# Optimization experiments

Measured on AMD Instinct MI355X. Metric: run time of the kernel, lower is better.

Reference implementation:

```python
import jax, jax.numpy as jnp
import numpy as np

N = 100000      # num_nodes
E = 600000      # edges per relation
R = 3           # num_relations
F_IN = 128
F_OUT = 64


def setup_inputs() -> dict:
    key = jax.random.key(0)
    k0, k1, k2, k3 = jax.random.split(key, 4)
    x = jax.random.normal(k0, (N, F_IN), dtype=jnp.float32)
    edge_indices = jax.random.randint(k1, (R, 2, E), 0, N, dtype=jnp.int32)
    # torch.randperm per relation -> fixed permutations as int inputs
    perms = jnp.stack([jax.random.permutation(jax.random.fold_in(k2, r), N).astype(jnp.int32)
                       for r in range(R)])
    # GCNConv glorot weight + zero bias, one per relation
    Ws = jax.random.normal(k3, (R, F_IN, F_OUT), dtype=jnp.float32) * (1.0 / np.sqrt(F_IN))
    bs = jnp.zeros((R, F_OUT), dtype=jnp.float32)
    return {"x": x, "edge_indices": edge_indices, "perms": perms, "Ws": Ws, "bs": bs}


def gcn_conv(h, src, dst, W, b, n):
    """PyG GCNConv: add self-loops, sym-normalize, linear, scatter-sum, bias."""
    loops = jnp.arange(n, dtype=src.dtype)
    s = jnp.concatenate([src, loops])
    d = jnp.concatenate([dst, loops])
    deg = jax.ops.segment_sum(jnp.ones_like(s, dtype=h.dtype), d, num_segments=n)
    dinv = jnp.where(deg > 0, jax.lax.rsqrt(deg), 0.0)
    norm = dinv[s] * dinv[d]                      # [E+n]
    hw = h @ W                                    # [n, F_OUT]
    out = jax.ops.segment_sum(hw[s] * norm[:, None], d, num_segments=n)
    return out + b


def reference(x, edge_indices, perms, Ws, bs):
    # Eval mode: F.dropout(p=0.5, training=False) is identity.
    n = x.shape[0]
    pos_hs, neg_hs, summaries = [], [], []
    for r in range(R):
        src, dst = edge_indices[r, 0], edge_indices[r, 1]
        pos_h = jax.nn.relu(gcn_conv(x, src, dst, Ws[r], bs[r], n))
        neg_h = jax.nn.relu(gcn_conv(x[perms[r]], src, dst, Ws[r], bs[r], n))
        pos_hs.append(pos_h)
        neg_hs.append(neg_h)
        summaries.append(pos_h.mean(axis=0, keepdims=True))
    return (jnp.stack(pos_hs), jnp.stack(neg_hs), jnp.stack(summaries))
```

## Files before the change

### kernel.cpp

```cpp
#include <hip/hip_runtime.h>

#define F_IN 128
#define F_OUT 64
#define NCHUNK 256

typedef float f32x2 __attribute__((ext_vector_type(2)));
typedef float f32x4 __attribute__((ext_vector_type(4)));
typedef short bf16x8 __attribute__((ext_vector_type(8)));

__device__ __forceinline__ unsigned short f2bf(float f) {
    unsigned int u = __float_as_uint(f);
    u += 0x7fff + ((u >> 16) & 1);
    return (unsigned short)(u >> 16);
}
__device__ __forceinline__ float bf2f(unsigned short s) {
    return __uint_as_float((unsigned int)s << 16);
}

__global__ __launch_bounds__(256) void prep_kernel(const int* __restrict__ ei,
                                                   const int* __restrict__ perm,
                                                   const float* __restrict__ W,
                                                   int* __restrict__ deg,
                                                   int* __restrict__ ip,
                                                   unsigned short* __restrict__ wt_hi,
                                                   unsigned short* __restrict__ wt_lo,
                                                   int N, int E, int R,
                                                   int degB, int invB) {
    int b = blockIdx.x;
    if (b < degB) {
        int idx = b * 256 + threadIdx.x;
        if (idx < R * E) {
            int r = idx / E, e = idx - r * E;
            int d = ei[(size_t)r * 2 * E + E + e];
            atomicAdd(&deg[(size_t)r * N + d], 1);
        }
    } else if (b < degB + invB) {
        int idx = (b - degB) * 256 + threadIdx.x;
        if (idx < R * N) {
            int r = idx / N, i = idx - r * N;
            ip[(size_t)r * N + perm[idx]] = i;
        }
    } else {
        int idx = (b - degB - invB) * 256 + threadIdx.x;
        if (idx < R * 64 * 128) {
            int k = idx & 127, c = (idx >> 7) & 63, r = idx >> 13;
            float v = W[((size_t)r * F_IN + k) * F_OUT + c];
            unsigned short h = f2bf(v);
            wt_hi[idx] = h;
            wt_lo[idx] = f2bf(v - bf2f(h));
        }
    }
}

__global__ __launch_bounds__(256) void scan_partial(const int* __restrict__ deg,
                                                    int* __restrict__ psum,
                                                    int N, int chunk) {
    int b = blockIdx.x;
    int r = b >> 8, c = b & 255;
    int start = c * chunk, end = min(start + chunk, N);
    int s = 0;
    for (int i = start + threadIdx.x; i < end; i += 256)
        s += deg[(size_t)r * N + i];
    __shared__ int ls[256];
    ls[threadIdx.x] = s;
    __syncthreads();
    for (int off = 128; off > 0; off >>= 1) {
        if (threadIdx.x < off) ls[threadIdx.x] += ls[threadIdx.x + off];
        __syncthreads();
    }
    if (threadIdx.x == 0) psum[b] = ls[0];
}

__global__ __launch_bounds__(256) void scan_apply2(int* __restrict__ deg,
                                                   const int* __restrict__ psum,
                                                   int* __restrict__ rowstart,
                                                   float* __restrict__ dinv,
                                                   int N, int chunk) {
    int b = blockIdx.x;
    int r = b >> 8, c = b & 255;
    int tid = threadIdx.x, lane = tid & 63, wv = tid >> 6;
    __shared__ int incl[256];
    __shared__ int wsum[4];

    int pv = psum[(r << 8) + tid];
    int sc = pv;
    #pragma unroll
    for (int off = 1; off < 64; off <<= 1) {
        int t = __shfl_up(sc, off, 64);
        if (lane >= off) sc += t;
    }
    if (lane == 63) wsum[wv] = sc;
    __syncthreads();
    int woff = 0;
    for (int w = 0; w < wv; ++w) woff += wsum[w];
    incl[tid] = woff + sc;
    __syncthreads();
    int base = (c == 0) ? 0 : incl[c - 1];
    if (c == 0 && tid == 0)
        rowstart[(size_t)r * (N + 1) + N] = incl[255];

    int start = c * chunk, end = min(start + chunk, N);
    int* dg = deg + (size_t)r * N;
    int* rs = rowstart + (size_t)r * (N + 1);
    float* dv = dinv + (size_t)r * N;
    int v[4]; int tsum = 0;
    #pragma unroll
    for (int j = 0; j < 4; ++j) {
        int idx = start + tid * 4 + j;
        v[j] = (idx < end) ? dg[idx] : 0;
        tsum += v[j];
    }
    int sc2 = tsum;
    #pragma unroll
    for (int off = 1; off < 64; off <<= 1) {
        int t = __shfl_up(sc2, off, 64);
        if (lane >= off) sc2 += t;
    }
    if (lane == 63) wsum[wv] = sc2;
    __syncthreads();
    int woff2 = 0;
    for (int w = 0; w < wv; ++w) woff2 += wsum[w];
    int excl = base + woff2 + sc2 - tsum;
    #pragma unroll
    for (int j = 0; j < 4; ++j) {
        int idx = start + tid * 4 + j;
        if (idx < end) {
            rs[idx] = excl;
            dg[idx] = excl;
            dv[idx] = rsqrtf((float)(v[j] + 1));
        }
        excl += v[j];
    }
}

__global__ __launch_bounds__(256) void fill_gemm(const int* __restrict__ ei,
                                                 const float* __restrict__ dinv,
                                                 int* __restrict__ cursor,
                                                 int2* __restrict__ csr,
                                                 const float* __restrict__ x,
                                                 const unsigned short* __restrict__ wt_hi,
                                                 const unsigned short* __restrict__ wt_lo,
                                                 const int* __restrict__ ip,
                                                 unsigned short* __restrict__ combined,
                                                 int N, int E, int R, int gemmB) {
    constexpr int KP = 136;
    __shared__ __align__(16) unsigned short xs_hi[64 * KP];
    __shared__ __align__(16) unsigned short xs_lo[64 * KP];
    int b = blockIdx.x;

    if (b >= gemmB) {
        int idx = (b - gemmB) * 256 + threadIdx.x;
        if (idx >= R * E) return;
        int r = idx / E, e = idx - r * E;
        const int* base = ei + (size_t)r * 2 * E;
        int s = base[e], d = base[E + e];
        const float* dv = dinv + (size_t)r * N;
        float nrm = dv[s] * dv[d];
        int pos = atomicAdd(&cursor[(size_t)r * N + d], 1);
        int2 sp; sp.x = s; sp.y = __float_as_int(nrm);
        csr[(size_t)r * E + pos] = sp;
        return;
    }

    int row0 = b * 64;
    int tid = threadIdx.x;
    {
        int rr = tid >> 2, q = tid & 3;
        int grow = row0 + rr; if (grow >= N) grow = N - 1;
        const float* xr = x + (size_t)grow * F_IN + q * 32;
        unsigned short* dh = &xs_hi[rr * KP + q * 32];
        unsigned short* dl = &xs_lo[rr * KP + q * 32];
        #pragma unroll
        for (int c = 0; c < 32; c += 4) {
            float4 v = *(const float4*)(xr + c);
            unsigned short h0 = f2bf(v.x), h1 = f2bf(v.y),
                           h2 = f2bf(v.z), h3 = f2bf(v.w);
            ushort4 hv; hv.x = h0; hv.y = h1; hv.z = h2; hv.w = h3;
            *(ushort4*)(dh + c) = hv;
            ushort4 lv;
            lv.x = f2bf(v.x - bf2f(h0)); lv.y = f2bf(v.y - bf2f(h1));
            lv.z = f2bf(v.z - bf2f(h2)); lv.w = f2bf(v.w - bf2f(h3));
            *(ushort4*)(dl + c) = lv;
        }
    }
    __syncthreads();

    int wv = tid >> 6, lane = tid & 63;
    int l15 = lane & 15, lhi = lane >> 4;
    int nbase = wv * 16;
    for (int r = 0; r < R; ++r) {
        f32x4 acc[4];
        #pragma unroll
        for (int ct = 0; ct < 4; ++ct) acc[ct] = (f32x4){0.f, 0.f, 0.f, 0.f};
        const unsigned short* wh = wt_hi + (size_t)r * 64 * 128;
        const unsigned short* wl = wt_lo + (size_t)r * 64 * 128;
        #pragma unroll
        for (int kc = 0; kc < 4; ++kc) {
            int kb = kc * 32 + lhi * 8;
            int ro = (nbase + l15) * KP + kb;
            bf16x8 bh = *(const bf16x8*)&xs_hi[ro];
            bf16x8 bl = *(const bf16x8*)&xs_lo[ro];
            bf16x8 ah[4], al[4];
            #pragma unroll
            for (int ct = 0; ct < 4; ++ct) {
                int wo = (ct * 16 + l15) * 128 + kb;
                ah[ct] = *(const bf16x8*)(wh + wo);
                al[ct] = *(const bf16x8*)(wl + wo);
            }
            #pragma unroll
            for (int ct = 0; ct < 4; ++ct) {
                acc[ct] = __builtin_amdgcn_mfma_f32_16x16x32_bf16(ah[ct], bh, acc[ct], 0, 0, 0);
                acc[ct] = __builtin_amdgcn_mfma_f32_16x16x32_bf16(ah[ct], bl, acc[ct], 0, 0, 0);
                acc[ct] = __builtin_amdgcn_mfma_f32_16x16x32_bf16(al[ct], bh, acc[ct], 0, 0, 0);
            }
        }
        const int* ipr = ip + (size_t)r * N;
        size_t rb = (size_t)r * N;
        int xrow = row0 + nbase + l15;
        if (xrow < N) {
            int nrow = ipr[xrow];
            #pragma unroll
            for (int ct = 0; ct < 4; ++ct) {
                f32x4 a = acc[ct];
                ushort4 v;
                v.x = f2bf(a.x); v.y = f2bf(a.y);
                v.z = f2bf(a.z); v.w = f2bf(a.w);
                int cb = ct * 16 + lhi * 4;
                *(ushort4*)(combined + (rb + xrow) * 128 + cb) = v;
                *(ushort4*)(combined + (rb + nrow) * 128 + 64 + cb) = v;
            }
        }
    }
}

__global__ __launch_bounds__(256) void gather_kernel(const int2* __restrict__ csr,
                                                     const int* __restrict__ rowstart,
                                                     const float* __restrict__ dinv,
                                                     const unsigned short* __restrict__ combined,
                                                     const float* __restrict__ bs,
                                                     float* __restrict__ out_pos,
                                                     float* __restrict__ out_neg,
                                                     float* __restrict__ partial,
                                                     int N, int E) {
    int r = blockIdx.y;
    int lane = threadIdx.x & 63, wv = threadIdx.x >> 6;
    int i = blockIdx.x * 4 + wv;
    i = __builtin_amdgcn_readfirstlane(i);
    int c0 = (lane & 31) * 2;
    __shared__ float ls[4][64];
    float p0 = 0.f, p1 = 0.f;
    if (i < N) {
        const unsigned short* cw = combined + (size_t)r * N * 128;
        const int* rs = rowstart + (size_t)r * (N + 1);
        int j0 = rs[i], j1 = rs[i + 1];
        j0 = __builtin_amdgcn_readfirstlane(j0);
        j1 = __builtin_amdgcn_readfirstlane(j1);
        float di = dinv[(size_t)r * N + i];
        float w = di * di;
        unsigned int sv = *(const unsigned int*)(cw + (size_t)i * 128 + 2 * lane);
        float acc0 = bf2f((unsigned short)sv) * w;
        float acc1 = bf2f((unsigned short)(sv >> 16)) * w;
        const int2* cs = csr + (size_t)r * E;
        int last = j1 - 1;
        for (int j = j0; j < j1; j += 8) {
            int2 e[8];
            float nm[8];
            #pragma unroll
            for (int k = 0; k < 8; ++k) {
                int idx = j + k;
                int ic = idx < last ? idx : last;
                e[k] = cs[ic];
                nm[k] = (idx < j1) ? __int_as_float(e[k].y) : 0.f;
            }
            #pragma unroll
            for (int k = 0; k < 8; ++k) {
                unsigned int v = *(const unsigned int*)(cw + (size_t)e[k].x * 128 + 2 * lane);
                acc0 += bf2f((unsigned short)v) * nm[k];
                acc1 += bf2f((unsigned short)(v >> 16)) * nm[k];
            }
        }
        float2 bv = *(const float2*)(bs + r * F_OUT + c0);
        float q0 = acc0 + bv.x; q0 = q0 > 0.f ? q0 : 0.f;
        float q1 = acc1 + bv.y; q1 = q1 > 0.f ? q1 : 0.f;
        size_t off = (size_t)r * N * F_OUT + (size_t)i * F_OUT + c0;
        float* dst = (lane < 32) ? (out_pos + off) : (out_neg + off);
        f32x2 o; o.x = q0; o.y = q1;
        __builtin_nontemporal_store(o, (f32x2*)dst);
        if (lane < 32) { p0 = q0; p1 = q1; }
    }
    if (lane < 32) { ls[wv][c0] = p0; ls[wv][c0 + 1] = p1; }
    __syncthreads();
    if (wv == 0) {
        float t = ls[0][lane] + ls[1][lane] + ls[2][lane] + ls[3][lane];
        atomicAdd(&partial[((size_t)r * 256 + (blockIdx.x & 255)) * F_OUT + lane], t);
    }
}

__global__ __launch_bounds__(256) void summary_reduce(const float* __restrict__ partial,
                                                      float* __restrict__ summary,
                                                      float inv_n) {
    int r = blockIdx.x;
    int lane = threadIdx.x & 63, wv = threadIdx.x >> 6;
    __shared__ float ls[256];
    float s = 0.f;
    for (int c = wv; c < 256; c += 4)
        s += partial[((size_t)r * 256 + c) * F_OUT + lane];
    ls[threadIdx.x] = s;
    __syncthreads();
    if (wv == 0)
        summary[r * F_OUT + lane] =
            (ls[lane] + ls[64 + lane] + ls[128 + lane] + ls[192 + lane]) * inv_n;
}

extern "C" void kernel_launch(void* const* d_in, const int* in_sizes, int n_in,
                              void* d_out, int out_size, void* d_ws, size_t ws_size,
                              hipStream_t stream) {
    const float* x    = (const float*)d_in[0];
    const int*   ei   = (const int*)d_in[1];
    const int*   perm = (const int*)d_in[2];
    const float* Ws   = (const float*)d_in[3];
    const float* bs   = (const float*)d_in[4];

    const int N = in_sizes[0] / F_IN;
    const int R = in_sizes[4] / F_OUT;
    const int E = in_sizes[1] / (2 * R);

    float* out_pos = (float*)d_out;
    float* out_neg = out_pos + (size_t)R * N * F_OUT;
    float* summary = out_neg + (size_t)R * N * F_OUT;

    char* ws = (char*)d_ws;
    size_t off = 0;
    auto alloc = [&](size_t bytes) { void* p = ws + off;
        off += (bytes + 255) & ~(size_t)255; return p; };
    int*   deg      = (int*)  alloc((size_t)R * N * 4);
    float* partial  = (float*)alloc((size_t)R * 256 * F_OUT * 4);
    float* dinv     = (float*)alloc((size_t)R * N * 4);
    int*   rowstart = (int*)  alloc((size_t)R * (N + 1) * 4);
    int*   ip       = (int*)  alloc((size_t)R * N * 4);
    int2*  csr      = (int2*) alloc((size_t)R * E * 8);
    unsigned short* combined = (unsigned short*)alloc((size_t)R * N * 128 * 2);
    int*   psum     = (int*)  alloc((size_t)R * NCHUNK * 4);
    unsigned short* wt_hi = (unsigned short*)alloc((size_t)R * 64 * 128 * 2);
    unsigned short* wt_lo = (unsigned short*)alloc((size_t)R * 64 * 128 * 2);

    const int chunk = (N + NCHUNK - 1) / NCHUNK;
    const int degB = (R * E + 255) / 256;
    const int invB = (R * N + 255) / 256;
    const int wB   = (R * 64 * 128 + 255) / 256;
    const int gemmB = (N + 63) / 64;

    size_t zbytes = (size_t)((char*)dinv - (char*)deg);
    hipMemsetAsync(deg, 0, zbytes, stream);

    prep_kernel<<<degB + invB + wB, 256, 0, stream>>>(ei, perm, Ws, deg, ip,
                                                      wt_hi, wt_lo, N, E, R,
                                                      degB, invB);
    scan_partial<<<R * NCHUNK, 256, 0, stream>>>(deg, psum, N, chunk);
    scan_apply2<<<R * NCHUNK, 256, 0, stream>>>(deg, psum, rowstart, dinv, N, chunk);
    fill_gemm<<<gemmB + degB, 256, 0, stream>>>(ei, dinv, deg, csr, x, wt_hi,
                                                wt_lo, ip, combined, N, E, R, gemmB);
    gather_kernel<<<dim3((N + 3) / 4, R), 256, 0, stream>>>(csr, rowstart, dinv,
                                                            combined, bs, out_pos,
                                                            out_neg, partial, N, E);
    summary_reduce<<<R, 256, 0, stream>>>(partial, summary, 1.0f / (float)N);
}
```

Before: 544.2 us.

## Record per-edge slot offsets during degree count to remove second atomic pass

```diff
diff --git a/kernel.cpp b/kernel.cpp
--- a/kernel.cpp
+++ b/kernel.cpp
@@ -21,6 +21,7 @@
                                                    const int* __restrict__ perm,
                                                    const float* __restrict__ W,
                                                    int* __restrict__ deg,
+                                                   int* __restrict__ eoff,
                                                    int* __restrict__ ip,
                                                    unsigned short* __restrict__ wt_hi,
                                                    unsigned short* __restrict__ wt_lo,
@@ -32,7 +33,8 @@
         if (idx < R * E) {
             int r = idx / E, e = idx - r * E;
             int d = ei[(size_t)r * 2 * E + E + e];
-            atomicAdd(&deg[(size_t)r * N + d], 1);
+            int pos = atomicAdd(&deg[(size_t)r * N + d], 1);
+            eoff[idx] = pos;
         }
     } else if (b < degB + invB) {
         int idx = (b - degB) * 256 + threadIdx.x;
@@ -71,7 +73,7 @@
     if (threadIdx.x == 0) psum[b] = ls[0];
 }
 
-__global__ __launch_bounds__(256) void scan_apply2(int* __restrict__ deg,
+__global__ __launch_bounds__(256) void scan_apply2(const int* __restrict__ deg,
                                                    const int* __restrict__ psum,
                                                    int* __restrict__ rowstart,
                                                    float* __restrict__ dinv,
@@ -100,7 +102,7 @@
         rowstart[(size_t)r * (N + 1) + N] = incl[255];
 
     int start = c * chunk, end = min(start + chunk, N);
-    int* dg = deg + (size_t)r * N;
+    const int* dg = deg + (size_t)r * N;
     int* rs = rowstart + (size_t)r * (N + 1);
     float* dv = dinv + (size_t)r * N;
     int v[4]; int tsum = 0;
@@ -126,43 +128,23 @@
         int idx = start + tid * 4 + j;
         if (idx < end) {
             rs[idx] = excl;
-            dg[idx] = excl;
             dv[idx] = rsqrtf((float)(v[j] + 1));
         }
         excl += v[j];
     }
 }
 
-__global__ __launch_bounds__(256) void fill_gemm(const int* __restrict__ ei,
-                                                 const float* __restrict__ dinv,
-                                                 int* __restrict__ cursor,
-                                                 int2* __restrict__ csr,
-                                                 const float* __restrict__ x,
-                                                 const unsigned short* __restrict__ wt_hi,
-                                                 const unsigned short* __restrict__ wt_lo,
-                                                 const int* __restrict__ ip,
-                                                 unsigned short* __restrict__ combined,
-                                                 int N, int E, int R, int gemmB) {
+__global__ __launch_bounds__(256) void gemm_xw(const float* __restrict__ x,
+                                               const unsigned short* __restrict__ wt_hi,
+                                               const unsigned short* __restrict__ wt_lo,
+                                               const int* __restrict__ ip,
+                                               unsigned short* __restrict__ combined,
+                                               int N, int R) {
     constexpr int KP = 136;
     __shared__ __align__(16) unsigned short xs_hi[64 * KP];
     __shared__ __align__(16) unsigned short xs_lo[64 * KP];
-    int b = blockIdx.x;
-
-    if (b >= gemmB) {
-        int idx = (b - gemmB) * 256 + threadIdx.x;
-        if (idx >= R * E) return;
-        int r = idx / E, e = idx - r * E;
-        const int* base = ei + (size_t)r * 2 * E;
-        int s = base[e], d = base[E + e];
-        const float* dv = dinv + (size_t)r * N;
-        float nrm = dv[s] * dv[d];
-        int pos = atomicAdd(&cursor[(size_t)r * N + d], 1);
-        int2 sp; sp.x = s; sp.y = __float_as_int(nrm);
-        csr[(size_t)r * E + pos] = sp;
-        return;
-    }
-
-    int row0 = b * 64;
+
+    int row0 = blockIdx.x * 64;
     int tid = threadIdx.x;
     {
         int rr = tid >> 2, q = tid & 3;
@@ -233,6 +215,24 @@
     }
 }
 
+__global__ __launch_bounds__(256) void fill_csr2(const int* __restrict__ ei,
+                                                 const int* __restrict__ eoff,
+                                                 const int* __restrict__ rowstart,
+                                                 const float* __restrict__ dinv,
+                                                 int2* __restrict__ csr,
+                                                 int N, int E, int R) {
+    int idx = blockIdx.x * 256 + threadIdx.x;
+    if (idx >= R * E) return;
+    int r = idx / E, e = idx - r * E;
+    const int* base = ei + (size_t)r * 2 * E;
+    int s = base[e], d = base[E + e];
+    const float* dv = dinv + (size_t)r * N;
+    float nrm = dv[s] * dv[d];
+    int pos = rowstart[(size_t)r * (N + 1) + d] + eoff[idx];
+    int2 sp; sp.x = s; sp.y = __float_as_int(nrm);
+    csr[(size_t)r * E + pos] = sp;
+}
+
 __global__ __launch_bounds__(256) void gather_kernel(const int2* __restrict__ csr,
                                                      const int* __restrict__ rowstart,
                                                      const float* __restrict__ dinv,
@@ -241,10 +241,11 @@
                                                      float* __restrict__ out_pos,
                                                      float* __restrict__ out_neg,
                                                      float* __restrict__ partial,
-                                                     int N, int E) {
-    int r = blockIdx.y;
+                                                     int N, int E, int perRel) {
+    int bid = blockIdx.x;
+    int r = bid / perRel, ib = bid - r * perRel;
     int lane = threadIdx.x & 63, wv = threadIdx.x >> 6;
-    int i = blockIdx.x * 4 + wv;
+    int i = ib * 4 + wv;
     i = __builtin_amdgcn_readfirstlane(i);
     int c0 = (lane & 31) * 2;
     __shared__ float ls[4][64];
@@ -292,7 +293,7 @@
     __syncthreads();
     if (wv == 0) {
         float t = ls[0][lane] + ls[1][lane] + ls[2][lane] + ls[3][lane];
-        atomicAdd(&partial[((size_t)r * 256 + (blockIdx.x & 255)) * F_OUT + lane], t);
+        atomicAdd(&partial[((size_t)r * 256 + (ib & 255)) * F_OUT + lane], t);
     }
 }
 
@@ -338,6 +339,7 @@
     float* dinv     = (float*)alloc((size_t)R * N * 4);
     int*   rowstart = (int*)  alloc((size_t)R * (N + 1) * 4);
     int*   ip       = (int*)  alloc((size_t)R * N * 4);
+    int*   eoff     = (int*)  alloc((size_t)R * E * 4);
     int2*  csr      = (int2*) alloc((size_t)R * E * 8);
     unsigned short* combined = (unsigned short*)alloc((size_t)R * N * 128 * 2);
     int*   psum     = (int*)  alloc((size_t)R * NCHUNK * 4);
@@ -349,19 +351,21 @@
     const int invB = (R * N + 255) / 256;
     const int wB   = (R * 64 * 128 + 255) / 256;
     const int gemmB = (N + 63) / 64;
+    const int perRel = (N + 3) / 4;
 
     size_t zbytes = (size_t)((char*)dinv - (char*)deg);
     hipMemsetAsync(deg, 0, zbytes, stream);
 
-    prep_kernel<<<degB + invB + wB, 256, 0, stream>>>(ei, perm, Ws, deg, ip,
-                                                      wt_hi, wt_lo, N, E, R,
+    prep_kernel<<<degB + invB + wB, 256, 0, stream>>>(ei, perm, Ws, deg, eoff,
+                                                      ip, wt_hi, wt_lo, N, E, R,
                                                       degB, invB);
     scan_partial<<<R * NCHUNK, 256, 0, stream>>>(deg, psum, N, chunk);
     scan_apply2<<<R * NCHUNK, 256, 0, stream>>>(deg, psum, rowstart, dinv, N, chunk);
-    fill_gemm<<<gemmB + degB, 256, 0, stream>>>(ei, dinv, deg, csr, x, wt_hi,
-                                                wt_lo, ip, combined, N, E, R, gemmB);
-    gather_kernel<<<dim3((N + 3) / 4, R), 256, 0, stream>>>(csr, rowstart, dinv,
-                                                            combined, bs, out_pos,
-                                                            out_neg, partial, N, E);
+    gemm_xw<<<gemmB, 256, 0, stream>>>(x, wt_hi, wt_lo, ip, combined, N, R);
+    fill_csr2<<<(R * E + 255) / 256, 256, 0, stream>>>(ei, eoff, rowstart, dinv,
+                                                       csr, N, E, R);
+    gather_kernel<<<perRel * R, 256, 0, stream>>>(csr, rowstart, dinv, combined,
+                                                  bs, out_pos, out_neg, partial,
+                                                  N, E, perRel);
     summary_reduce<<<R, 256, 0, stream>>>(partial, summary, 1.0f / (float)N);
 }
```

Result: faster. 529.6 us (-2.7%).
